# Kernel optimization log

Hardware: AMD Instinct MI355X
Metric: run time of the kernel (lower is better)

## Reference

```python
import jax, jax.numpy as jnp
import numpy as np

B = 4          # num_batches
R = 128        # resolution per axis (cubic grid)
N = 4_194_304  # total sample points
EMA_DECAY = 0.95


def setup_inputs() -> dict:
    key = jax.random.key(0)
    k1, k2, k3, k4 = jax.random.split(key, 4)
    occ_val_grid = jax.random.uniform(k1, (B, R, R, R), dtype=jnp.float32)
    pts = jax.random.uniform(k2, (N, 3), minval=-1.0, maxval=1.0, dtype=jnp.float32)
    occ_val = jax.random.uniform(k3, (N,), dtype=jnp.float32)
    bidx = jax.random.randint(k4, (N,), 0, B, dtype=jnp.int32)
    return dict(occ_val_grid=occ_val_grid, pts=pts, occ_val=occ_val, bidx=bidx)


def reference(occ_val_grid, pts, occ_val, bidx):
    """Faithful port of update_batched_occ_val_grid_ (bidx path):
    1) quantize normalized pts in [-1,1] to integer voxel coords, clamped;
    2) ravel (bidx, gx, gy, gz) -> flat index;
    3) scatter_max of occ_val into an EMA-decayed copy of the grid;
    4) write back only at the touched indices (index_put_), so untouched
       voxels keep their OLD, non-decayed value."""
    res = jnp.array([R, R, R], dtype=jnp.int32)
    # ((pts/2 + 0.5) * res).long().clamp(0, res-1)
    gidx = ((pts / 2.0 + 0.5) * res.astype(pts.dtype)).astype(jnp.int32)
    gidx = jnp.clip(gidx, 0, res - 1)                      # [N, 3]
    strides = jnp.array([R * R, R, 1], dtype=jnp.int32)
    idx_ravel = bidx * (R * R * R) + (gidx * strides).sum(-1)  # [N]

    flat = occ_val_grid.reshape(-1)                        # [B*R^3]
    decayed = EMA_DECAY * flat                             # scatter_max 'out' buffer
    occ_val_new = decayed.at[idx_ravel].max(occ_val)       # scatter_max with out=decayed
    # index_put_ writeback: only touched voxels get the new (decayed/maxed) value
    out = flat.at[idx_ravel].set(occ_val_new[idx_ravel])
    return out.reshape(B, R, R, R)
```

## Files before the change

### kernel.cpp

```cpp
#include <hip/hip_runtime.h>
#include <hip/hip_bf16.h>


#define GRID_R          128
#define EMA_DEC         0.95f
#define NBUCKET         512
#define VOX_PER_BUCKET  16384
#define PTS_PER_BLOCK   4096
#define PTS_PER_THREAD  16

__device__ __forceinline__ int quant_clamp(float p) {
    int g = (int)((p * 0.5f + 0.5f) * (float)GRID_R);
    return min(max(g, 0), GRID_R - 1);
}

__global__ __launch_bounds__(256)
void occ_localsort_kernel(const float* __restrict__ pts,
                          const float* __restrict__ occ_val,
                          const int*   __restrict__ bidx,
                          unsigned*        __restrict__ sorted,
                          unsigned short*  __restrict__ offT,
                          int n_total, int nchunk) {
    __shared__ unsigned rec[PTS_PER_BLOCK];
    __shared__ int      cur[NBUCKET];
    __shared__ int      wsum[4];

    const int tid  = threadIdx.x;
    const int lane = tid & 63;
    const int wv   = tid >> 6;
    const int c    = blockIdx.x;

    for (int b = tid; b < NBUCKET; b += 256) cur[b] = 0;
    __syncthreads();

    const float4* pts4 = reinterpret_cast<const float4*>(pts);
    const float4* ov4  = reinterpret_cast<const float4*>(occ_val);
    const int4*   bi4  = reinterpret_cast<const int4*>(bidx);

    int pk[PTS_PER_THREAD];
    int bk[PTS_PER_THREAD];

    #pragma unroll
    for (int r = 0; r < PTS_PER_THREAD / 8; ++r) {
        const int i = c * ((PTS_PER_THREAD / 8) * 256) + r * 256 + tid;
        if (i * 8 + 7 < n_total) {
            float4 q0 = pts4[i * 6 + 0];
            float4 q1 = pts4[i * 6 + 1];
            float4 q2 = pts4[i * 6 + 2];
            float4 q3 = pts4[i * 6 + 3];
            float4 q4 = pts4[i * 6 + 4];
            float4 q5 = pts4[i * 6 + 5];
            float4 oa = ov4[i * 2 + 0];
            float4 ob = ov4[i * 2 + 1];
            int4   ba = bi4[i * 2 + 0];
            int4   bb = bi4[i * 2 + 1];

            float xs[8] = {q0.x, q0.w, q1.z, q2.y, q3.x, q3.w, q4.z, q5.y};
            float ys[8] = {q0.y, q1.x, q1.w, q2.z, q3.y, q4.x, q4.w, q5.z};
            float zs[8] = {q0.z, q1.y, q2.x, q2.w, q3.z, q4.y, q5.x, q5.w};
            int   vb[8] = {__float_as_int(oa.x), __float_as_int(oa.y),
                           __float_as_int(oa.z), __float_as_int(oa.w),
                           __float_as_int(ob.x), __float_as_int(ob.y),
                           __float_as_int(ob.z), __float_as_int(ob.w)};
            int   bs[8] = {ba.x, ba.y, ba.z, ba.w, bb.x, bb.y, bb.z, bb.w};

            #pragma unroll
            for (int k = 0; k < 8; ++k) {
                int gx = quant_clamp(xs[k]);
                int gy = quant_clamp(ys[k]);
                int gz = quant_clamp(zs[k]);
                int idx = bs[k] * (GRID_R * GRID_R * GRID_R)
                        + gx * (GRID_R * GRID_R) + gy * GRID_R + gz;
                pk[r * 8 + k] = (vb[k] & (int)0xFFFFC000) | (idx & 0x3FFF);
                bk[r * 8 + k] = idx >> 14;
            }
        } else {
            #pragma unroll
            for (int k = 0; k < 8; ++k) {
                bk[r * 8 + k] = -1;
                pk[r * 8 + k] = 0;
                int p = i * 8 + k;
                if (p < n_total) {
                    int gx = quant_clamp(pts[p * 3 + 0]);
                    int gy = quant_clamp(pts[p * 3 + 1]);
                    int gz = quant_clamp(pts[p * 3 + 2]);
                    int idx = bidx[p] * (GRID_R * GRID_R * GRID_R)
                            + gx * (GRID_R * GRID_R) + gy * GRID_R + gz;
                    pk[r * 8 + k] = (__float_as_int(occ_val[p]) & (int)0xFFFFC000)
                                  | (idx & 0x3FFF);
                    bk[r * 8 + k] = idx >> 14;
                }
            }
        }
    }

    #pragma unroll
    for (int k = 0; k < PTS_PER_THREAD; ++k)
        if (bk[k] >= 0) atomicAdd(&cur[bk[k]], 1);
    __syncthreads();

    const int a = cur[2 * tid];
    const int cc = cur[2 * tid + 1];
    const int s = a + cc;
    int x = s;
    #pragma unroll
    for (int off = 1; off < 64; off <<= 1) {
        int v = __shfl_up(x, off, 64);
        if (lane >= off) x += v;
    }
    if (lane == 63) wsum[wv] = x;
    __syncthreads();

    const int w0 = wsum[0], w1 = wsum[1], w2 = wsum[2], w3 = wsum[3];
    const int wofs  = (wv > 0 ? w0 : 0) + (wv > 1 ? w1 : 0) + (wv > 2 ? w2 : 0);
    const int total = w0 + w1 + w2 + w3;
    const int excl  = x + wofs - s;

    offT[(size_t)(2 * tid)     * nchunk + c] = (unsigned short)excl;
    offT[(size_t)(2 * tid + 1) * nchunk + c] = (unsigned short)(excl + a);
    if (tid == 255)
        offT[(size_t)NBUCKET   * nchunk + c] = (unsigned short)total;

    cur[2 * tid]     = excl;
    cur[2 * tid + 1] = excl + a;
    __syncthreads();

    #pragma unroll
    for (int k = 0; k < PTS_PER_THREAD; ++k) {
        if (bk[k] >= 0) {
            int slot = atomicAdd(&cur[bk[k]], 1);
            rec[slot] = (unsigned)pk[k];
        }
    }
    __syncthreads();

    unsigned* dst = sorted + (size_t)c * PTS_PER_BLOCK;
    for (int j = tid; j < total; j += 256)
        dst[j] = rec[j];
}

__global__ __launch_bounds__(512)
void occ_bucket5_kernel(const unsigned*       __restrict__ sorted,
                        const unsigned short* __restrict__ offT,
                        const float*          __restrict__ grid,
                        float*                __restrict__ out,
                        int nchunk) {
    __shared__ int smax[VOX_PER_BUCKET];
    const int tid = threadIdx.x;
    const int b = (blockIdx.x & 7) * (NBUCKET / 8) + (blockIdx.x >> 3);

    int4* s4 = reinterpret_cast<int4*>(smax);
    for (int j = tid; j < VOX_PER_BUCKET / 4; j += 512)
        s4[j] = make_int4(-1, -1, -1, -1);
    __syncthreads();

    const unsigned short* rowLo = offT + (size_t)b       * nchunk;
    const unsigned short* rowHi = offT + (size_t)(b + 1) * nchunk;

    for (int c = tid; c < nchunk; c += 512) {
        const int lo = rowLo[c];
        const int hi = rowHi[c];
        const unsigned* rp = sorted + (size_t)c * PTS_PER_BLOCK;
        for (int j = (lo & ~3); j < hi; j += 4) {
            uint4 e = *reinterpret_cast<const uint4*>(rp + j);
            if (j     >= lo && j     < hi)
                atomicMax(&smax[e.x & (VOX_PER_BUCKET - 1)], (int)e.x);
            if (j + 1 >= lo && j + 1 < hi)
                atomicMax(&smax[e.y & (VOX_PER_BUCKET - 1)], (int)e.y);
            if (j + 2 >= lo && j + 2 < hi)
                atomicMax(&smax[e.z & (VOX_PER_BUCKET - 1)], (int)e.z);
            if (j + 3 >= lo && j + 3 < hi)
                atomicMax(&smax[e.w & (VOX_PER_BUCKET - 1)], (int)e.w);
        }
    }
    __syncthreads();

    const size_t vbase = (size_t)b * VOX_PER_BUCKET;
    const float4* g4  = reinterpret_cast<const float4*>(grid + vbase);
    float4*       o4  = reinterpret_cast<float4*>(out + vbase);
    const int4*   sm4 = reinterpret_cast<const int4*>(smax);
    for (int j = tid; j < VOX_PER_BUCKET / 4; j += 512) {
        int4   w = sm4[j];
        float4 g = g4[j];
        float4 r;
        r.x = (w.x == -1) ? g.x
            : fmaxf(EMA_DEC * g.x, __int_as_float(w.x & (int)0xFFFFC000));
        r.y = (w.y == -1) ? g.y
            : fmaxf(EMA_DEC * g.y, __int_as_float(w.y & (int)0xFFFFC000));
        r.z = (w.z == -1) ? g.z
            : fmaxf(EMA_DEC * g.z, __int_as_float(w.z & (int)0xFFFFC000));
        r.w = (w.w == -1) ? g.w
            : fmaxf(EMA_DEC * g.w, __int_as_float(w.w & (int)0xFFFFC000));
        o4[j] = r;
    }
}

__global__ void occ_scatter8_kernel(const float* __restrict__ pts,
                                    const float* __restrict__ occ_val,
                                    const int*   __restrict__ bidx,
                                    int*         __restrict__ out_bits,
                                    int n8, int n_total) {
    const int tid    = blockIdx.x * blockDim.x + threadIdx.x;
    const int stride = gridDim.x * blockDim.x;

    const float4* pts4 = reinterpret_cast<const float4*>(pts);
    const float4* ov4  = reinterpret_cast<const float4*>(occ_val);
    const int4*   bi4  = reinterpret_cast<const int4*>(bidx);

    for (int i = tid; i < n8; i += stride) {
        float4 q0 = pts4[i * 6 + 0];
        float4 q1 = pts4[i * 6 + 1];
        float4 q2 = pts4[i * 6 + 2];
        float4 q3 = pts4[i * 6 + 3];
        float4 q4 = pts4[i * 6 + 4];
        float4 q5 = pts4[i * 6 + 5];
        float4 oa = ov4[i * 2 + 0];
        float4 ob = ov4[i * 2 + 1];
        int4   ba = bi4[i * 2 + 0];
        int4   bb = bi4[i * 2 + 1];

        float xs[8] = {q0.x, q0.w, q1.z, q2.y, q3.x, q3.w, q4.z, q5.y};
        float ys[8] = {q0.y, q1.x, q1.w, q2.z, q3.y, q4.x, q4.w, q5.z};
        float zs[8] = {q0.z, q1.y, q2.x, q2.w, q3.z, q4.y, q5.x, q5.w};
        int   vb[8] = {__float_as_int(oa.x), __float_as_int(oa.y),
                       __float_as_int(oa.z), __float_as_int(oa.w),
                       __float_as_int(ob.x), __float_as_int(ob.y),
                       __float_as_int(ob.z), __float_as_int(ob.w)};
        int   bs[8] = {ba.x, ba.y, ba.z, ba.w, bb.x, bb.y, bb.z, bb.w};

        int idx[8];
        #pragma unroll
        for (int k = 0; k < 8; ++k) {
            int gx = quant_clamp(xs[k]);
            int gy = quant_clamp(ys[k]);
            int gz = quant_clamp(zs[k]);
            idx[k] = bs[k] * (GRID_R * GRID_R * GRID_R)
                   + gx * (GRID_R * GRID_R) + gy * GRID_R + gz;
        }
        #pragma unroll
        for (int k = 0; k < 8; ++k) atomicMax(&out_bits[idx[k]], vb[k]);
    }

    for (int i = n8 * 8 + tid; i < n_total; i += stride) {
        int gx = quant_clamp(pts[i * 3 + 0]);
        int gy = quant_clamp(pts[i * 3 + 1]);
        int gz = quant_clamp(pts[i * 3 + 2]);
        int idx = bidx[i] * (GRID_R * GRID_R * GRID_R)
                + gx * (GRID_R * GRID_R) + gy * GRID_R + gz;
        atomicMax(&out_bits[idx], __float_as_int(occ_val[i]));
    }
}

__global__ void occ_finalize_kernel(const float* __restrict__ grid,
                                    float*       __restrict__ out,
                                    int v4, int v_total) {
    const int tid    = blockIdx.x * blockDim.x + threadIdx.x;
    const int stride = gridDim.x * blockDim.x;

    const float4* g4 = reinterpret_cast<const float4*>(grid);
    int4*         w4 = reinterpret_cast<int4*>(out);
    float4*       o4 = reinterpret_cast<float4*>(out);

    for (int i = tid; i < v4; i += stride) {
        int4   w = w4[i];
        float4 g = g4[i];
        float4 r;
        r.x = (w.x == -1) ? g.x : fmaxf(EMA_DEC * g.x, __int_as_float(w.x));
        r.y = (w.y == -1) ? g.y : fmaxf(EMA_DEC * g.y, __int_as_float(w.y));
        r.z = (w.z == -1) ? g.z : fmaxf(EMA_DEC * g.z, __int_as_float(w.z));
        r.w = (w.w == -1) ? g.w : fmaxf(EMA_DEC * g.w, __int_as_float(w.w));
        o4[i] = r;
    }
    for (int i = v4 * 4 + tid; i < v_total; i += stride) {
        int w = reinterpret_cast<int*>(out)[i];
        float g = grid[i];
        out[i] = (w == -1) ? g : fmaxf(EMA_DEC * g, __int_as_float(w));
    }
}

extern "C" void kernel_launch(void* const* d_in, const int* in_sizes, int n_in,
                              void* d_out, int out_size, void* d_ws, size_t ws_size,
                              hipStream_t stream) {
    const float* grid    = (const float*)d_in[0];
    const float* pts     = (const float*)d_in[1];
    const float* occ_val = (const float*)d_in[2];
    const int*   bidx    = (const int*)d_in[3];

    float* out = (float*)d_out;
    const int N = in_sizes[2];

    const int nchunk = (N + PTS_PER_BLOCK - 1) / PTS_PER_BLOCK;

    const size_t sorted_b = (size_t)nchunk * PTS_PER_BLOCK * sizeof(unsigned);
    const size_t off_b    = (size_t)(NBUCKET + 1) * nchunk * sizeof(unsigned short);
    const size_t need     = sorted_b + off_b + 16;
    const bool shape_ok   = (out_size == 4 * GRID_R * GRID_R * GRID_R);

    if (ws_size >= need && shape_ok && nchunk >= 1) {
        unsigned*       sorted = (unsigned*)d_ws;
        unsigned short* offT   = (unsigned short*)((char*)d_ws + sorted_b);

        occ_localsort_kernel<<<nchunk, 256, 0, stream>>>(
            pts, occ_val, bidx, sorted, offT, N, nchunk);
        occ_bucket5_kernel<<<NBUCKET, 512, 0, stream>>>(
            sorted, offT, grid, out, nchunk);
    } else {
        hipMemsetAsync(d_out, 0xFF, (size_t)out_size * sizeof(float), stream);

        const int n8 = N / 8;
        int sblocks = (n8 + 255) / 256;
        if (sblocks < 1) sblocks = 1;
        occ_scatter8_kernel<<<sblocks, 256, 0, stream>>>(
            pts, occ_val, bidx, (int*)d_out, n8, N);

        const int v4 = out_size / 4;
        int fblocks = (v4 + 255) / 256;
        if (fblocks > 2048) fblocks = 2048;
        if (fblocks < 1) fblocks = 1;
        occ_finalize_kernel<<<fblocks, 256, 0, stream>>>(grid, out, v4, out_size);
    }
}
```

Measured before the change: 43.78 us.

## Enlarge sort chunks, scatter ranks directly to global, split bucket rows across threads

The local-sort kernel now uses 1024 threads and 16384-point chunks, so there are four times fewer chunks. It drops the shared-memory staging buffer and writes each record straight to its global slot, with the prefix scan done by 512 threads over 8 waves. The bucket kernel moves to 1024 threads and assigns four threads per chunk row, interleaving uint4 reads. The goal is to shrink the offset table and the per-bucket chunk loop and to raise parallelism in the atomicMax phase. In exchange, the global writes are scattered and uncoalesced, and occupancy may drop with larger blocks.

```diff
diff --git a/kernel.cpp b/kernel.cpp
--- a/kernel.cpp
+++ b/kernel.cpp
@@ -6,7 +6,8 @@
 #define EMA_DEC         0.95f
 #define NBUCKET         512
 #define VOX_PER_BUCKET  16384
-#define PTS_PER_BLOCK   4096
+#define PTS_PER_BLOCK   16384
+#define K1_THREADS      1024
 #define PTS_PER_THREAD  16
 
 __device__ __forceinline__ int quant_clamp(float p) {
@@ -14,23 +15,22 @@
     return min(max(g, 0), GRID_R - 1);
 }
 
-__global__ __launch_bounds__(256)
-void occ_localsort_kernel(const float* __restrict__ pts,
-                          const float* __restrict__ occ_val,
-                          const int*   __restrict__ bidx,
-                          unsigned*        __restrict__ sorted,
-                          unsigned short*  __restrict__ offT,
-                          int n_total, int nchunk) {
-    __shared__ unsigned rec[PTS_PER_BLOCK];
-    __shared__ int      cur[NBUCKET];
-    __shared__ int      wsum[4];
+__global__ __launch_bounds__(1024)
+void occ_localsort3_kernel(const float* __restrict__ pts,
+                           const float* __restrict__ occ_val,
+                           const int*   __restrict__ bidx,
+                           unsigned*        __restrict__ sorted,
+                           unsigned short*  __restrict__ offT,
+                           int n_total, int nchunk) {
+    __shared__ int cur[NBUCKET];
+    __shared__ int wsum[8];
 
     const int tid  = threadIdx.x;
     const int lane = tid & 63;
     const int wv   = tid >> 6;
     const int c    = blockIdx.x;
 
-    for (int b = tid; b < NBUCKET; b += 256) cur[b] = 0;
+    for (int b = tid; b < NBUCKET; b += K1_THREADS) cur[b] = 0;
     __syncthreads();
 
     const float4* pts4 = reinterpret_cast<const float4*>(pts);
@@ -42,7 +42,8 @@
 
     #pragma unroll
     for (int r = 0; r < PTS_PER_THREAD / 8; ++r) {
-        const int i = c * ((PTS_PER_THREAD / 8) * 256) + r * 256 + tid;
+        const int i = c * ((PTS_PER_THREAD / 8) * K1_THREADS)
+                    + r * K1_THREADS + tid;
         if (i * 8 + 7 < n_total) {
             float4 q0 = pts4[i * 6 + 0];
             float4 q1 = pts4[i * 6 + 1];
@@ -99,48 +100,46 @@
         if (bk[k] >= 0) atomicAdd(&cur[bk[k]], 1);
     __syncthreads();
 
-    const int a = cur[2 * tid];
-    const int cc = cur[2 * tid + 1];
-    const int s = a + cc;
-    int x = s;
-    #pragma unroll
-    for (int off = 1; off < 64; off <<= 1) {
-        int v = __shfl_up(x, off, 64);
-        if (lane >= off) x += v;
-    }
-    if (lane == 63) wsum[wv] = x;
-    __syncthreads();
-
-    const int w0 = wsum[0], w1 = wsum[1], w2 = wsum[2], w3 = wsum[3];
-    const int wofs  = (wv > 0 ? w0 : 0) + (wv > 1 ? w1 : 0) + (wv > 2 ? w2 : 0);
-    const int total = w0 + w1 + w2 + w3;
-    const int excl  = x + wofs - s;
-
-    offT[(size_t)(2 * tid)     * nchunk + c] = (unsigned short)excl;
-    offT[(size_t)(2 * tid + 1) * nchunk + c] = (unsigned short)(excl + a);
-    if (tid == 255)
-        offT[(size_t)NBUCKET   * nchunk + c] = (unsigned short)total;
-
-    cur[2 * tid]     = excl;
-    cur[2 * tid + 1] = excl + a;
-    __syncthreads();
-
+    int a = 0, x = 0;
+    if (tid < NBUCKET) {
+        a = cur[tid];
+        x = a;
+        #pragma unroll
+        for (int off = 1; off < 64; off <<= 1) {
+            int v = __shfl_up(x, off, 64);
+            if (lane >= off) x += v;
+        }
+        if (lane == 63) wsum[wv] = x;
+    }
+    __syncthreads();
+
+    if (tid < NBUCKET) {
+        int wofs = 0;
+        #pragma unroll
+        for (int w = 0; w < 8; ++w) if (w < wv) wofs += wsum[w];
+        const int excl = x + wofs - a;
+        offT[(size_t)tid * nchunk + c] = (unsigned short)excl;
+        cur[tid] = excl;
+        if (tid == 0) {
+            int total = wsum[0] + wsum[1] + wsum[2] + wsum[3]
+                      + wsum[4] + wsum[5] + wsum[6] + wsum[7];
+            offT[(size_t)NBUCKET * nchunk + c] = (unsigned short)total;
+        }
+    }
+    __syncthreads();
+
+    unsigned* dst = sorted + (size_t)c * PTS_PER_BLOCK;
     #pragma unroll
     for (int k = 0; k < PTS_PER_THREAD; ++k) {
         if (bk[k] >= 0) {
-            int slot = atomicAdd(&cur[bk[k]], 1);
-            rec[slot] = (unsigned)pk[k];
-        }
-    }
-    __syncthreads();
-
-    unsigned* dst = sorted + (size_t)c * PTS_PER_BLOCK;
-    for (int j = tid; j < total; j += 256)
-        dst[j] = rec[j];
-}
-
-__global__ __launch_bounds__(512)
-void occ_bucket5_kernel(const unsigned*       __restrict__ sorted,
+            int rank = atomicAdd(&cur[bk[k]], 1);
+            dst[rank] = (unsigned)pk[k];
+        }
+    }
+}
+
+__global__ __launch_bounds__(1024)
+void occ_bucket7_kernel(const unsigned*       __restrict__ sorted,
                         const unsigned short* __restrict__ offT,
                         const float*          __restrict__ grid,
                         float*                __restrict__ out,
@@ -150,18 +149,20 @@
     const int b = (blockIdx.x & 7) * (NBUCKET / 8) + (blockIdx.x >> 3);
 
     int4* s4 = reinterpret_cast<int4*>(smax);
-    for (int j = tid; j < VOX_PER_BUCKET / 4; j += 512)
+    for (int j = tid; j < VOX_PER_BUCKET / 4; j += 1024)
         s4[j] = make_int4(-1, -1, -1, -1);
     __syncthreads();
 
     const unsigned short* rowLo = offT + (size_t)b       * nchunk;
     const unsigned short* rowHi = offT + (size_t)(b + 1) * nchunk;
 
-    for (int c = tid; c < nchunk; c += 512) {
+    for (int t = tid; t < nchunk * 4; t += 1024) {
+        const int c  = t >> 2;
+        const int p  = t & 3;
         const int lo = rowLo[c];
         const int hi = rowHi[c];
         const unsigned* rp = sorted + (size_t)c * PTS_PER_BLOCK;
-        for (int j = (lo & ~3); j < hi; j += 4) {
+        for (int j = (lo & ~3) + 4 * p; j < hi; j += 16) {
             uint4 e = *reinterpret_cast<const uint4*>(rp + j);
             if (j     >= lo && j     < hi)
                 atomicMax(&smax[e.x & (VOX_PER_BUCKET - 1)], (int)e.x);
@@ -179,7 +180,7 @@
     const float4* g4  = reinterpret_cast<const float4*>(grid + vbase);
     float4*       o4  = reinterpret_cast<float4*>(out + vbase);
     const int4*   sm4 = reinterpret_cast<const int4*>(smax);
-    for (int j = tid; j < VOX_PER_BUCKET / 4; j += 512) {
+    for (int j = tid; j < VOX_PER_BUCKET / 4; j += 1024) {
         int4   w = sm4[j];
         float4 g = g4[j];
         float4 r;
@@ -296,13 +297,13 @@
     const size_t need     = sorted_b + off_b + 16;
     const bool shape_ok   = (out_size == 4 * GRID_R * GRID_R * GRID_R);
 
-    if (ws_size >= need && shape_ok && nchunk >= 1) {
+    if (ws_size >= need && shape_ok && nchunk >= 1 && nchunk < 65536) {
         unsigned*       sorted = (unsigned*)d_ws;
         unsigned short* offT   = (unsigned short*)((char*)d_ws + sorted_b);
 
-        occ_localsort_kernel<<<nchunk, 256, 0, stream>>>(
+        occ_localsort3_kernel<<<nchunk, K1_THREADS, 0, stream>>>(
             pts, occ_val, bidx, sorted, offT, N, nchunk);
-        occ_bucket5_kernel<<<NBUCKET, 512, 0, stream>>>(
+        occ_bucket7_kernel<<<NBUCKET, 1024, 0, stream>>>(
             sorted, offT, grid, out, nchunk);
     } else {
         hipMemsetAsync(d_out, 0xFF, (size_t)out_size * sizeof(float), stream);
```

After: 72.80 us. 1.66x slower.

## Add merge pass combining four local-sorted chunks into super-segments before bucket max

Applied to the files above, without the earlier changes.

Adds an intermediate kernel that merges bucket-sorted records from groups of four chunks into larger contiguous super-segments with a combined offset table. The bucket kernel then walks 256 super-segments instead of 1024 chunks, and its block size rises to 1024 with four threads sharing each segment. The aim is to cut short scattered per-chunk reads and offset lookups in the bucket pass. The cost is an extra launch and an extra read and write of the whole sorted array, plus narrower shape conditions for taking the fast path. An unused bkt shared array is also written in the sort kernel.

```diff
diff --git a/kernel.cpp b/kernel.cpp
--- a/kernel.cpp
+++ b/kernel.cpp
@@ -6,8 +6,10 @@
 #define EMA_DEC         0.95f
 #define NBUCKET         512
 #define VOX_PER_BUCKET  16384
-#define PTS_PER_BLOCK   4096
+#define CH              4096
 #define PTS_PER_THREAD  16
+#define SUPER           4
+#define SSEG            (CH * SUPER)
 
 __device__ __forceinline__ int quant_clamp(float p) {
     int g = (int)((p * 0.5f + 0.5f) * (float)GRID_R);
@@ -21,9 +23,10 @@
                           unsigned*        __restrict__ sorted,
                           unsigned short*  __restrict__ offT,
                           int n_total, int nchunk) {
-    __shared__ unsigned rec[PTS_PER_BLOCK];
-    __shared__ int      cur[NBUCKET];
-    __shared__ int      wsum[4];
+    __shared__ unsigned       rec[CH];
+    __shared__ unsigned short bkt[CH];
+    __shared__ int            cur[NBUCKET];
+    __shared__ int            wsum[4];
 
     const int tid  = threadIdx.x;
     const int lane = tid & 63;
@@ -99,9 +102,9 @@
         if (bk[k] >= 0) atomicAdd(&cur[bk[k]], 1);
     __syncthreads();
 
-    const int a = cur[2 * tid];
+    const int a  = cur[2 * tid];
     const int cc = cur[2 * tid + 1];
-    const int s = a + cc;
+    const int s  = a + cc;
     int x = s;
     #pragma unroll
     for (int off = 1; off < 64; off <<= 1) {
@@ -130,38 +133,91 @@
         if (bk[k] >= 0) {
             int slot = atomicAdd(&cur[bk[k]], 1);
             rec[slot] = (unsigned)pk[k];
+            bkt[slot] = (unsigned short)bk[k];
         }
     }
     __syncthreads();
 
-    unsigned* dst = sorted + (size_t)c * PTS_PER_BLOCK;
+    unsigned* dst = sorted + (size_t)c * CH;
     for (int j = tid; j < total; j += 256)
         dst[j] = rec[j];
 }
 
-__global__ __launch_bounds__(512)
-void occ_bucket5_kernel(const unsigned*       __restrict__ sorted,
+__global__ __launch_bounds__(1024)
+void occ_merge_kernel(const unsigned*       __restrict__ src,
+                      const unsigned short* __restrict__ offT,
+                      unsigned*             __restrict__ merged,
+                      unsigned short*       __restrict__ offT2,
+                      int nchunk, int nsuper) {
+    extern __shared__ unsigned srcs[];
+    __shared__ unsigned short colOff[SUPER][NBUCKET + 1];
+
+    const int tid = threadIdx.x;
+    const int s   = blockIdx.x;
+    const int c0  = s * SUPER;
+
+    {
+        const uint4* g4 = reinterpret_cast<const uint4*>(src + (size_t)c0 * CH);
+        uint4* l4 = reinterpret_cast<uint4*>(srcs);
+        for (int j = tid; j < SSEG / 4; j += 1024)
+            l4[j] = g4[j];
+    }
+
+    for (int t = tid; t <= NBUCKET; t += 1024) {
+        const unsigned short* p = offT + (size_t)t * nchunk + c0;
+        ushort4 v = *reinterpret_cast<const ushort4*>(p);
+        colOff[0][t] = v.x;
+        colOff[1][t] = v.y;
+        colOff[2][t] = v.z;
+        colOff[3][t] = v.w;
+    }
+    __syncthreads();
+
+    for (int t = tid; t <= NBUCKET; t += 1024)
+        offT2[(size_t)t * nsuper + s] = (unsigned short)
+            (colOff[0][t] + colOff[1][t] + colOff[2][t] + colOff[3][t]);
+
+    unsigned* dst = merged + (size_t)s * SSEG;
+    for (int pair = tid; pair < NBUCKET * SUPER; pair += 1024) {
+        const int b  = pair >> 2;
+        const int i  = pair & 3;
+        const int lo = colOff[i][b];
+        const int hi = colOff[i][b + 1];
+        int m = colOff[0][b] + colOff[1][b] + colOff[2][b] + colOff[3][b];
+        #pragma unroll
+        for (int j = 0; j < SUPER; ++j)
+            if (j < i) m += colOff[j][b + 1] - colOff[j][b];
+        const unsigned* sp = srcs + i * CH;
+        for (int j = lo; j < hi; ++j)
+            dst[m + (j - lo)] = sp[j];
+    }
+}
+
+__global__ __launch_bounds__(1024)
+void occ_bucket7_kernel(const unsigned*       __restrict__ sorted,
                         const unsigned short* __restrict__ offT,
                         const float*          __restrict__ grid,
                         float*                __restrict__ out,
-                        int nchunk) {
+                        int nseg) {
     __shared__ int smax[VOX_PER_BUCKET];
     const int tid = threadIdx.x;
     const int b = (blockIdx.x & 7) * (NBUCKET / 8) + (blockIdx.x >> 3);
 
     int4* s4 = reinterpret_cast<int4*>(smax);
-    for (int j = tid; j < VOX_PER_BUCKET / 4; j += 512)
+    for (int j = tid; j < VOX_PER_BUCKET / 4; j += 1024)
         s4[j] = make_int4(-1, -1, -1, -1);
     __syncthreads();
 
-    const unsigned short* rowLo = offT + (size_t)b       * nchunk;
-    const unsigned short* rowHi = offT + (size_t)(b + 1) * nchunk;
-
-    for (int c = tid; c < nchunk; c += 512) {
+    const unsigned short* rowLo = offT + (size_t)b       * nseg;
+    const unsigned short* rowHi = offT + (size_t)(b + 1) * nseg;
+
+    for (int t = tid; t < nseg * 4; t += 1024) {
+        const int c  = t >> 2;
+        const int p  = t & 3;
         const int lo = rowLo[c];
         const int hi = rowHi[c];
-        const unsigned* rp = sorted + (size_t)c * PTS_PER_BLOCK;
-        for (int j = (lo & ~3); j < hi; j += 4) {
+        const unsigned* rp = sorted + (size_t)c * SSEG;
+        for (int j = (lo & ~3) + 4 * p; j < hi; j += 16) {
             uint4 e = *reinterpret_cast<const uint4*>(rp + j);
             if (j     >= lo && j     < hi)
                 atomicMax(&smax[e.x & (VOX_PER_BUCKET - 1)], (int)e.x);
@@ -179,7 +235,7 @@
     const float4* g4  = reinterpret_cast<const float4*>(grid + vbase);
     float4*       o4  = reinterpret_cast<float4*>(out + vbase);
     const int4*   sm4 = reinterpret_cast<const int4*>(smax);
-    for (int j = tid; j < VOX_PER_BUCKET / 4; j += 512) {
+    for (int j = tid; j < VOX_PER_BUCKET / 4; j += 1024) {
         int4   w = sm4[j];
         float4 g = g4[j];
         float4 r;
@@ -289,21 +345,31 @@
     float* out = (float*)d_out;
     const int N = in_sizes[2];
 
-    const int nchunk = (N + PTS_PER_BLOCK - 1) / PTS_PER_BLOCK;
-
-    const size_t sorted_b = (size_t)nchunk * PTS_PER_BLOCK * sizeof(unsigned);
-    const size_t off_b    = (size_t)(NBUCKET + 1) * nchunk * sizeof(unsigned short);
-    const size_t need     = sorted_b + off_b + 16;
+    const int nchunk = (N + CH - 1) / CH;
+    const int nsuper = nchunk / SUPER;
+
+    const size_t src_b    = (size_t)nchunk * CH * sizeof(unsigned);
+    const size_t merged_b = (size_t)nsuper * SSEG * sizeof(unsigned);
+    const size_t offT_b   = (size_t)(NBUCKET + 1) * nchunk * sizeof(unsigned short);
+    const size_t offT2_b  = (size_t)(NBUCKET + 1) * nsuper * sizeof(unsigned short);
+    const size_t need     = src_b + merged_b + offT_b + offT2_b + 32;
     const bool shape_ok   = (out_size == 4 * GRID_R * GRID_R * GRID_R);
-
-    if (ws_size >= need && shape_ok && nchunk >= 1) {
-        unsigned*       sorted = (unsigned*)d_ws;
-        unsigned short* offT   = (unsigned short*)((char*)d_ws + sorted_b);
+    const bool grid_ok    = (nchunk >= 4) && (nchunk % SUPER == 0)
+                         && (nchunk <= 1024);
+
+    if (ws_size >= need && shape_ok && grid_ok) {
+        unsigned*       src    = (unsigned*)d_ws;
+        unsigned*       merged = (unsigned*)((char*)d_ws + src_b);
+        unsigned short* offT   = (unsigned short*)((char*)d_ws + src_b + merged_b);
+        unsigned short* offT2  = (unsigned short*)((char*)d_ws + src_b + merged_b
+                                                   + offT_b);
 
         occ_localsort_kernel<<<nchunk, 256, 0, stream>>>(
-            pts, occ_val, bidx, sorted, offT, N, nchunk);
-        occ_bucket5_kernel<<<NBUCKET, 512, 0, stream>>>(
-            sorted, offT, grid, out, nchunk);
+            pts, occ_val, bidx, src, offT, N, nchunk);
+        occ_merge_kernel<<<nsuper, 1024, SSEG * sizeof(unsigned), stream>>>(
+            src, offT, merged, offT2, nchunk, nsuper);
+        occ_bucket7_kernel<<<NBUCKET, 1024, 0, stream>>>(
+            merged, offT2, grid, out, nsuper);
     } else {
         hipMemsetAsync(d_out, 0xFF, (size_t)out_size * sizeof(float), stream);
 
```

After: 50.78 us. +16.0%, slower.

## Halve bucket count to 256 with 32K-voxel LDS tiles and 1024-thread bucket blocks

Applied to the files above, without the earlier changes.

Re-partitions the voxel grid into 256 buckets of 32768 voxels, so each bucket block holds a 128KB LDS max-table and runs 1024 threads. Four threads now share each chunk's bucket segment, interleaving uint4 reads. The local sort does a simpler one-bucket-per-thread scan. To fit the larger in-bucket voxel index, one more mantissa bit of occ_val is dropped from the packed key, which slightly coarsens the stored max values. The large LDS allocation also limits each CU to one bucket block.

```diff
diff --git a/kernel.cpp b/kernel.cpp
--- a/kernel.cpp
+++ b/kernel.cpp
@@ -4,9 +4,9 @@
 
 #define GRID_R          128
 #define EMA_DEC         0.95f
-#define NBUCKET         512
-#define VOX_PER_BUCKET  16384
-#define PTS_PER_BLOCK   4096
+#define NBUCKET         256
+#define VOX_PER_BUCKET  32768
+#define CH              4096
 #define PTS_PER_THREAD  16
 
 __device__ __forceinline__ int quant_clamp(float p) {
@@ -15,13 +15,13 @@
 }
 
 __global__ __launch_bounds__(256)
-void occ_localsort_kernel(const float* __restrict__ pts,
-                          const float* __restrict__ occ_val,
-                          const int*   __restrict__ bidx,
-                          unsigned*        __restrict__ sorted,
-                          unsigned short*  __restrict__ offT,
-                          int n_total, int nchunk) {
-    __shared__ unsigned rec[PTS_PER_BLOCK];
+void occ_localsort256_kernel(const float* __restrict__ pts,
+                             const float* __restrict__ occ_val,
+                             const int*   __restrict__ bidx,
+                             unsigned*        __restrict__ sorted,
+                             unsigned short*  __restrict__ offT,
+                             int n_total, int nchunk) {
+    __shared__ unsigned rec[CH];
     __shared__ int      cur[NBUCKET];
     __shared__ int      wsum[4];
 
@@ -30,7 +30,7 @@
     const int wv   = tid >> 6;
     const int c    = blockIdx.x;
 
-    for (int b = tid; b < NBUCKET; b += 256) cur[b] = 0;
+    cur[tid] = 0;
     __syncthreads();
 
     const float4* pts4 = reinterpret_cast<const float4*>(pts);
@@ -71,8 +71,8 @@
                 int gz = quant_clamp(zs[k]);
                 int idx = bs[k] * (GRID_R * GRID_R * GRID_R)
                         + gx * (GRID_R * GRID_R) + gy * GRID_R + gz;
-                pk[r * 8 + k] = (vb[k] & (int)0xFFFFC000) | (idx & 0x3FFF);
-                bk[r * 8 + k] = idx >> 14;
+                pk[r * 8 + k] = (vb[k] & (int)0xFFFF8000) | (idx & 0x7FFF);
+                bk[r * 8 + k] = idx >> 15;
             }
         } else {
             #pragma unroll
@@ -86,9 +86,9 @@
                     int gz = quant_clamp(pts[p * 3 + 2]);
                     int idx = bidx[p] * (GRID_R * GRID_R * GRID_R)
                             + gx * (GRID_R * GRID_R) + gy * GRID_R + gz;
-                    pk[r * 8 + k] = (__float_as_int(occ_val[p]) & (int)0xFFFFC000)
-                                  | (idx & 0x3FFF);
-                    bk[r * 8 + k] = idx >> 14;
+                    pk[r * 8 + k] = (__float_as_int(occ_val[p]) & (int)0xFFFF8000)
+                                  | (idx & 0x7FFF);
+                    bk[r * 8 + k] = idx >> 15;
                 }
             }
         }
@@ -99,10 +99,8 @@
         if (bk[k] >= 0) atomicAdd(&cur[bk[k]], 1);
     __syncthreads();
 
-    const int a = cur[2 * tid];
-    const int cc = cur[2 * tid + 1];
-    const int s = a + cc;
-    int x = s;
+    const int a = cur[tid];
+    int x = a;
     #pragma unroll
     for (int off = 1; off < 64; off <<= 1) {
         int v = __shfl_up(x, off, 64);
@@ -114,15 +112,12 @@
     const int w0 = wsum[0], w1 = wsum[1], w2 = wsum[2], w3 = wsum[3];
     const int wofs  = (wv > 0 ? w0 : 0) + (wv > 1 ? w1 : 0) + (wv > 2 ? w2 : 0);
     const int total = w0 + w1 + w2 + w3;
-    const int excl  = x + wofs - s;
-
-    offT[(size_t)(2 * tid)     * nchunk + c] = (unsigned short)excl;
-    offT[(size_t)(2 * tid + 1) * nchunk + c] = (unsigned short)(excl + a);
+    const int excl  = x + wofs - a;
+
+    offT[(size_t)tid * nchunk + c] = (unsigned short)excl;
     if (tid == 255)
-        offT[(size_t)NBUCKET   * nchunk + c] = (unsigned short)total;
-
-    cur[2 * tid]     = excl;
-    cur[2 * tid + 1] = excl + a;
+        offT[(size_t)NBUCKET * nchunk + c] = (unsigned short)total;
+    cur[tid] = excl;
     __syncthreads();
 
     #pragma unroll
@@ -134,34 +129,36 @@
     }
     __syncthreads();
 
-    unsigned* dst = sorted + (size_t)c * PTS_PER_BLOCK;
+    unsigned* dst = sorted + (size_t)c * CH;
     for (int j = tid; j < total; j += 256)
         dst[j] = rec[j];
 }
 
-__global__ __launch_bounds__(512)
-void occ_bucket5_kernel(const unsigned*       __restrict__ sorted,
-                        const unsigned short* __restrict__ offT,
-                        const float*          __restrict__ grid,
-                        float*                __restrict__ out,
-                        int nchunk) {
+__global__ __launch_bounds__(1024)
+void occ_bucket2x_kernel(const unsigned*       __restrict__ sorted,
+                         const unsigned short* __restrict__ offT,
+                         const float*          __restrict__ grid,
+                         float*                __restrict__ out,
+                         int nchunk) {
     __shared__ int smax[VOX_PER_BUCKET];
     const int tid = threadIdx.x;
     const int b = (blockIdx.x & 7) * (NBUCKET / 8) + (blockIdx.x >> 3);
 
     int4* s4 = reinterpret_cast<int4*>(smax);
-    for (int j = tid; j < VOX_PER_BUCKET / 4; j += 512)
+    for (int j = tid; j < VOX_PER_BUCKET / 4; j += 1024)
         s4[j] = make_int4(-1, -1, -1, -1);
     __syncthreads();
 
     const unsigned short* rowLo = offT + (size_t)b       * nchunk;
     const unsigned short* rowHi = offT + (size_t)(b + 1) * nchunk;
 
-    for (int c = tid; c < nchunk; c += 512) {
+    for (int t = tid; t < nchunk * 4; t += 1024) {
+        const int c  = t >> 2;
+        const int p  = t & 3;
         const int lo = rowLo[c];
         const int hi = rowHi[c];
-        const unsigned* rp = sorted + (size_t)c * PTS_PER_BLOCK;
-        for (int j = (lo & ~3); j < hi; j += 4) {
+        const unsigned* rp = sorted + (size_t)c * CH;
+        for (int j = (lo & ~3) + 4 * p; j < hi; j += 16) {
             uint4 e = *reinterpret_cast<const uint4*>(rp + j);
             if (j     >= lo && j     < hi)
                 atomicMax(&smax[e.x & (VOX_PER_BUCKET - 1)], (int)e.x);
@@ -179,18 +176,18 @@
     const float4* g4  = reinterpret_cast<const float4*>(grid + vbase);
     float4*       o4  = reinterpret_cast<float4*>(out + vbase);
     const int4*   sm4 = reinterpret_cast<const int4*>(smax);
-    for (int j = tid; j < VOX_PER_BUCKET / 4; j += 512) {
+    for (int j = tid; j < VOX_PER_BUCKET / 4; j += 1024) {
         int4   w = sm4[j];
         float4 g = g4[j];
         float4 r;
         r.x = (w.x == -1) ? g.x
-            : fmaxf(EMA_DEC * g.x, __int_as_float(w.x & (int)0xFFFFC000));
+            : fmaxf(EMA_DEC * g.x, __int_as_float(w.x & (int)0xFFFF8000));
         r.y = (w.y == -1) ? g.y
-            : fmaxf(EMA_DEC * g.y, __int_as_float(w.y & (int)0xFFFFC000));
+            : fmaxf(EMA_DEC * g.y, __int_as_float(w.y & (int)0xFFFF8000));
         r.z = (w.z == -1) ? g.z
-            : fmaxf(EMA_DEC * g.z, __int_as_float(w.z & (int)0xFFFFC000));
+            : fmaxf(EMA_DEC * g.z, __int_as_float(w.z & (int)0xFFFF8000));
         r.w = (w.w == -1) ? g.w
-            : fmaxf(EMA_DEC * g.w, __int_as_float(w.w & (int)0xFFFFC000));
+            : fmaxf(EMA_DEC * g.w, __int_as_float(w.w & (int)0xFFFF8000));
         o4[j] = r;
     }
 }
@@ -289,20 +286,20 @@
     float* out = (float*)d_out;
     const int N = in_sizes[2];
 
-    const int nchunk = (N + PTS_PER_BLOCK - 1) / PTS_PER_BLOCK;
-
-    const size_t sorted_b = (size_t)nchunk * PTS_PER_BLOCK * sizeof(unsigned);
+    const int nchunk = (N + CH - 1) / CH;
+
+    const size_t sorted_b = (size_t)nchunk * CH * sizeof(unsigned);
     const size_t off_b    = (size_t)(NBUCKET + 1) * nchunk * sizeof(unsigned short);
     const size_t need     = sorted_b + off_b + 16;
     const bool shape_ok   = (out_size == 4 * GRID_R * GRID_R * GRID_R);
 
-    if (ws_size >= need && shape_ok && nchunk >= 1) {
+    if (ws_size >= need && shape_ok && nchunk >= 1 && nchunk < 65536) {
         unsigned*       sorted = (unsigned*)d_ws;
         unsigned short* offT   = (unsigned short*)((char*)d_ws + sorted_b);
 
-        occ_localsort_kernel<<<nchunk, 256, 0, stream>>>(
+        occ_localsort256_kernel<<<nchunk, 256, 0, stream>>>(
             pts, occ_val, bidx, sorted, offT, N, nchunk);
-        occ_bucket5_kernel<<<NBUCKET, 512, 0, stream>>>(
+        occ_bucket2x_kernel<<<NBUCKET, 1024, 0, stream>>>(
             sorted, offT, grid, out, nchunk);
     } else {
         hipMemsetAsync(d_out, 0xFF, (size_t)out_size * sizeof(float), stream);
```

New measurement: 39.54 us. -9.7%, faster.
